# Kernel tuning notes

Measured on AMD Instinct MI355X. Metric: run time of the kernel, lower is better.

The kernel has to match this reference:

```python
import jax, jax.numpy as jnp
import numpy as np

N, M, D = 4096, 4096, 8

def laplace_tensor_markov(x, grid, lengthscale):
    # product over dims of exp(-|x_i - y_j|/ls) == exp(-sum_d |x_id - y_jd|/ls_d)
    # x: [n,d], grid: [m,d] -> [n,m]
    diff = jnp.abs(x[:, None, :] - grid[None, :, :]) / lengthscale  # [n,m,d]
    return jnp.exp(-jnp.sum(diff, axis=-1))

def setup_inputs() -> dict:
    key = jax.random.key(0)
    k1, k2, k3 = jax.random.split(key, 3)
    x = jax.random.normal(k1, (N, D), dtype=jnp.float32)
    sparse_grid = jax.random.uniform(k2, (M, D), dtype=jnp.float32)
    # inverse Cholesky factor is lower-triangular; emulate its structured sparsity
    L = jax.random.normal(k3, (M, M), dtype=jnp.float32) * 0.02
    chol_inv = jnp.tril(L) + jnp.eye(M, dtype=jnp.float32)
    lengthscale = jnp.ones((D,), dtype=jnp.float32)
    return {"x": x, "sparse_grid": sparse_grid, "chol_inv": chol_inv, "lengthscale": lengthscale}

def reference(x, sparse_grid, chol_inv, lengthscale):
    k_star = laplace_tensor_markov(x, sparse_grid, lengthscale)  # [n,m]
    phi = k_star @ chol_inv                                      # [n,m]
    return phi
```

## Files before the change

### kernel.cpp

```cpp
#include <hip/hip_runtime.h>
#include <cstdint>
#include <cstddef>

typedef unsigned short u16;
typedef __bf16 bf16x8 __attribute__((ext_vector_type(8)));
typedef float floatx4 __attribute__((ext_vector_type(4)));

#define NPTS 4096
#define MGRD 4096
#define DDIM 8

static __device__ __forceinline__ u16 f2bf(float f) {
    uint32_t u = __float_as_uint(f);
    u += 0x7fffu + ((u >> 16) & 1u);
    return (u16)(u >> 16);
}

__global__ __launch_bounds__(256) void prep_kernel(
    const float* __restrict__ x, const float* __restrict__ g,
    const float* __restrict__ ls, const float* __restrict__ B,
    u16* __restrict__ A, u16* __restrict__ Bt)
{
    __shared__ float tile[64][65];
    const int bid = blockIdx.x;
    const int tid = threadIdx.x;

    if (bid < 512) {
        const int kb = bid & 1;
        const int n0 = (bid >> 1) * 16;
        const int k0 = kb * 2048 + tid * 8;

        float il[DDIM];
#pragma unroll
        for (int d = 0; d < DDIM; ++d) il[d] = 1.0f / ls[d];

        float4 g0[8], g1[8];
#pragma unroll
        for (int r = 0; r < 8; ++r) {
            g0[r] = *reinterpret_cast<const float4*>(g + (size_t)(k0 + r) * DDIM);
            g1[r] = *reinterpret_cast<const float4*>(g + (size_t)(k0 + r) * DDIM + 4);
        }

        for (int nn = 0; nn < 16; ++nn) {
            const int n = n0 + nn;
            const float4 x0 = *reinterpret_cast<const float4*>(x + (size_t)n * DDIM);
            const float4 x1 = *reinterpret_cast<const float4*>(x + (size_t)n * DDIM + 4);
            alignas(16) u16 res[8];
#pragma unroll
            for (int r = 0; r < 8; ++r) {
                float s = fabsf(x0.x - g0[r].x) * il[0] + fabsf(x0.y - g0[r].y) * il[1]
                        + fabsf(x0.z - g0[r].z) * il[2] + fabsf(x0.w - g0[r].w) * il[3]
                        + fabsf(x1.x - g1[r].x) * il[4] + fabsf(x1.y - g1[r].y) * il[5]
                        + fabsf(x1.z - g1[r].z) * il[6] + fabsf(x1.w - g1[r].w) * il[7];
                res[r] = f2bf(__expf(-s));
            }
            *reinterpret_cast<uint4*>(A + (size_t)n * MGRD + k0) =
                *reinterpret_cast<const uint4*>(res);
        }
    } else {
        const int id = bid - 512;
        const int bx = id & 63;
        const int by = id >> 6;
        if (by < (bx & ~1)) return;
        const int k0 = by * 64;
        const int m0 = bx * 64;

#pragma unroll
        for (int r = 0; r < 4; ++r) {
            int c   = r * 256 + tid;
            int row = c >> 4;
            int col = (c & 15) * 4;
            const float4 v = *reinterpret_cast<const float4*>(&B[(size_t)(k0 + row) * MGRD + m0 + col]);
            tile[row][col + 0] = v.x; tile[row][col + 1] = v.y;
            tile[row][col + 2] = v.z; tile[row][col + 3] = v.w;
        }
        __syncthreads();

#pragma unroll
        for (int r = 0; r < 2; ++r) {
            int c  = r * 256 + tid;
            int mr = c >> 3;
            int kc = (c & 7) * 8;
            alignas(16) u16 tmp[8];
#pragma unroll
            for (int j = 0; j < 8; ++j)
                tmp[j] = f2bf(tile[kc + j][mr]);
            *reinterpret_cast<uint4*>(&Bt[(size_t)(m0 + mr) * MGRD + k0 + kc]) =
                *reinterpret_cast<const uint4*>(tmp);
        }
    }
}


#define FENCE() asm volatile("" ::: "memory")
static __device__ __forceinline__ void bar() {
    FENCE(); __builtin_amdgcn_s_barrier(); FENCE();
}

__global__ __launch_bounds__(512, 2) void gemm_pair_kernel(
    const u16* __restrict__ A,
    const u16* __restrict__ Bt,
    float* __restrict__ C)
{
    __shared__ u16 lds[3 * 24576] __attribute__((aligned(16)));

    const int tid  = threadIdx.x;
    const int lane = tid & 63;
    const int w    = tid >> 6;
    const int kg   = w >> 2;
    const int wq   = w & 3;
    const int nq   = wq >> 1;
    const int mq   = wq & 1;
    const int lrow = lane & 15;
    const int lhi  = lane >> 4;
    const int r7   = lrow & 7;

    const int id  = blockIdx.x;
    const int bm1 = id >> 4;
    const int bn  = id & 15;
    const int bn0 = bn << 8;

    const int arow = tid >> 3;
    const int aswz = ((tid ^ arow) & 7) * 8;
    int aoff[4];
#pragma unroll
    for (int r = 0; r < 4; ++r)
        aoff[r] = (bn0 + r * 64 + arow) * 4096 + aswz;

    const int ldst = w * 512;
    const int cswz = ((kg * 4 + lhi) ^ r7) * 8;
    const int rowA = (nq * 128 + lrow) * 64 + cswz;
    const int rowB = (mq * 64  + lrow) * 64 + cswz;

#define STG_A(QA, R, K) __builtin_amdgcn_global_load_lds(                        \
    (const __attribute__((address_space(1))) void*)(A + (size_t)aoff[R] + (K)),  \
    (__attribute__((address_space(3))) void*)((QA) + (R) * 4096 + ldst), 16, 0, 0)
#define STG_B(QB, R, K) __builtin_amdgcn_global_load_lds(                        \
    (const __attribute__((address_space(1))) void*)(Bt + (size_t)boff[R] + (K)), \
    (__attribute__((address_space(3))) void*)((QB) + (R) * 4096 + ldst), 16, 0, 0)

    bf16x8 af[8], bfv[4];

    floatx4 acc[8][4];

#define MF(a, b, c) __builtin_amdgcn_mfma_f32_16x16x32_bf16(a, b, c, 0, 0, 0)
#define MFMA32() do {                                                            \
    __builtin_amdgcn_s_setprio(1);                                               \
    _Pragma("unroll")                                                            \
    for (int i_ = 0; i_ < 8; ++i_)                                               \
        _Pragma("unroll")                                                        \
        for (int j_ = 0; j_ < 4; ++j_)                                           \
            acc[i_][j_] = MF(af[i_], bfv[j_], acc[i_][j_]);                      \
    __builtin_amdgcn_s_setprio(0);                                               \
} while (0)

#define REGION(PA, PB, QA, QB, KST) do {                                         \
    STG_A(QA, 0, KST); STG_A(QA, 1, KST);                                        \
    af[0]  = *reinterpret_cast<const bf16x8*>((PA) + rowA + 0 * 1024);           \
    bfv[0] = *reinterpret_cast<const bf16x8*>((PB) + rowB + 0 * 1024);           \
    bfv[1] = *reinterpret_cast<const bf16x8*>((PB) + rowB + 1 * 1024);           \
    bfv[2] = *reinterpret_cast<const bf16x8*>((PB) + rowB + 2 * 1024);           \
    bfv[3] = *reinterpret_cast<const bf16x8*>((PB) + rowB + 3 * 1024);           \
    STG_A(QA, 2, KST); STG_A(QA, 3, KST);                                        \
    af[1]  = *reinterpret_cast<const bf16x8*>((PA) + rowA + 1 * 1024);           \
    af[2]  = *reinterpret_cast<const bf16x8*>((PA) + rowA + 2 * 1024);           \
    af[3]  = *reinterpret_cast<const bf16x8*>((PA) + rowA + 3 * 1024);           \
    STG_B(QB, 0, KST); STG_B(QB, 1, KST);                                        \
    af[4]  = *reinterpret_cast<const bf16x8*>((PA) + rowA + 4 * 1024);           \
    af[5]  = *reinterpret_cast<const bf16x8*>((PA) + rowA + 5 * 1024);           \
    af[6]  = *reinterpret_cast<const bf16x8*>((PA) + rowA + 6 * 1024);           \
    af[7]  = *reinterpret_cast<const bf16x8*>((PA) + rowA + 7 * 1024);           \
    MFMA32();                                                                    \
} while (0)

#define RDALL(PA, PB) do {                                                       \
    af[0]  = *reinterpret_cast<const bf16x8*>((PA) + rowA + 0 * 1024);           \
    bfv[0] = *reinterpret_cast<const bf16x8*>((PB) + rowB + 0 * 1024);           \
    bfv[1] = *reinterpret_cast<const bf16x8*>((PB) + rowB + 1 * 1024);           \
    bfv[2] = *reinterpret_cast<const bf16x8*>((PB) + rowB + 2 * 1024);           \
    bfv[3] = *reinterpret_cast<const bf16x8*>((PB) + rowB + 3 * 1024);           \
    af[1]  = *reinterpret_cast<const bf16x8*>((PA) + rowA + 1 * 1024);           \
    af[2]  = *reinterpret_cast<const bf16x8*>((PA) + rowA + 2 * 1024);           \
    af[3]  = *reinterpret_cast<const bf16x8*>((PA) + rowA + 3 * 1024);           \
    af[4]  = *reinterpret_cast<const bf16x8*>((PA) + rowA + 4 * 1024);           \
    af[5]  = *reinterpret_cast<const bf16x8*>((PA) + rowA + 5 * 1024);           \
    af[6]  = *reinterpret_cast<const bf16x8*>((PA) + rowA + 6 * 1024);           \
    af[7]  = *reinterpret_cast<const bf16x8*>((PA) + rowA + 7 * 1024);           \
} while (0)

    for (int jj = 0; jj < 2; ++jj) {
        const int bm  = jj ? (31 - bm1) : bm1;
        const int bm0 = bm << 7;
        const int L   = 64 - 2 * bm;

        int boff[2];
#pragma unroll
        for (int r = 0; r < 2; ++r)
            boff[r] = (bm0 + r * 64 + arow) * 4096 + aswz;

#pragma unroll
        for (int i = 0; i < 8; ++i)
#pragma unroll
            for (int j = 0; j < 4; ++j)
                acc[i][j] = (floatx4)0.0f;

        int kT = 4096 - 64;
        {
            u16* qA0 = lds;             u16* qB0 = lds + 16384;
            u16* qA1 = lds + 24576;     u16* qB1 = lds + 24576 + 16384;
            STG_A(qA0, 0, kT); STG_A(qA0, 1, kT); STG_A(qA0, 2, kT); STG_A(qA0, 3, kT);
            STG_B(qB0, 0, kT); STG_B(qB0, 1, kT);
            STG_A(qA1, 0, kT - 64); STG_A(qA1, 1, kT - 64);
            STG_A(qA1, 2, kT - 64); STG_A(qA1, 3, kT - 64);
            STG_B(qB1, 0, kT - 64); STG_B(qB1, 1, kT - 64);
        }
        asm volatile("s_waitcnt vmcnt(6)" ::: "memory");
        bar();

        int p = 0;
        for (int T = 0; T < L - 2; ++T) {
            u16* pA = lds + p * 24576;  u16* pB = pA + 16384;
            int p2 = p + 2; if (p2 >= 3) p2 -= 3;
            u16* qA = lds + p2 * 24576; u16* qB = qA + 16384;

            REGION(pA, pB, qA, qB, kT - 128);
            asm volatile("s_waitcnt vmcnt(6)" ::: "memory");
            bar();

            kT -= 64; ++p; if (p == 3) p = 0;
        }

        {
            u16* pA = lds + p * 24576;  u16* pB = pA + 16384;
            RDALL(pA, pB);
            MFMA32();
            asm volatile("s_waitcnt vmcnt(0)" ::: "memory");
            bar();
            ++p; if (p == 3) p = 0;
        }
        {
            u16* pA = lds + p * 24576;  u16* pB = pA + 16384;
            RDALL(pA, pB);
            MFMA32();
        }

        __syncthreads();
        float* scr = reinterpret_cast<float*>(lds);
        if (kg == 1) {
#pragma unroll
            for (int i = 0; i < 8; ++i)
#pragma unroll
                for (int j = 0; j < 4; ++j)
                    *reinterpret_cast<floatx4*>(
                        scr + (size_t)wq * 8192 + (i * 4 + j) * 256 + lane * 4) = acc[i][j];
        }
        __syncthreads();
        if (kg == 0) {
#pragma unroll
            for (int i = 0; i < 8; ++i)
#pragma unroll
                for (int j = 0; j < 4; ++j)
                    acc[i][j] += *reinterpret_cast<const floatx4*>(
                        scr + (size_t)wq * 8192 + (i * 4 + j) * 256 + lane * 4);

#pragma unroll
            for (int i = 0; i < 8; ++i) {
                int rown = bn0 + nq * 128 + i * 16 + lhi * 4;
#pragma unroll
                for (int j = 0; j < 4; ++j) {
                    int colm = bm0 + mq * 64 + j * 16 + lrow;
                    float* cp = C + (size_t)rown * 4096 + colm;
#pragma unroll
                    for (int rr = 0; rr < 4; ++rr)
                        cp[(size_t)rr * 4096] = acc[i][j][rr];
                }
            }
        }
        __syncthreads();
    }
}

extern "C" void kernel_launch(void* const* d_in, const int* in_sizes, int n_in,
                              void* d_out, int out_size, void* d_ws, size_t ws_size,
                              hipStream_t stream)
{
    const float* x    = (const float*)d_in[0];
    const float* grid = (const float*)d_in[1];
    const float* ci   = (const float*)d_in[2];
    const float* ls   = (const float*)d_in[3];
    float* out = (float*)d_out;

    u16* wsA  = (u16*)d_ws;
    u16* wsBt = (u16*)d_ws + (size_t)MGRD * MGRD;

    prep_kernel<<<dim3(512 + 64 * 64), 256, 0, stream>>>(x, grid, ls, ci, wsA, wsBt);
    gemm_pair_kernel<<<dim3(256), 512, 0, stream>>>(wsA, wsBt, out);
}
```

Measured before the change: 185.1 us.

## Fuse prep and GEMM into one cooperative persistent kernel with grid sync

```diff
diff --git a/kernel.cpp b/kernel.cpp
--- a/kernel.cpp
+++ b/kernel.cpp
@@ -1,6 +1,9 @@
 #include <hip/hip_runtime.h>
+#include <hip/hip_cooperative_groups.h>
 #include <cstdint>
 #include <cstddef>
+
+namespace cg = cooperative_groups;
 
 typedef unsigned short u16;
 typedef __bf16 bf16x8 __attribute__((ext_vector_type(8)));
@@ -9,6 +12,9 @@
 #define NPTS 4096
 #define MGRD 4096
 #define DDIM 8
+
+#define AS1 __attribute__((address_space(1)))
+#define AS3 __attribute__((address_space(3)))
 
 static __device__ __forceinline__ u16 f2bf(float f) {
     uint32_t u = __float_as_uint(f);
@@ -16,19 +22,32 @@
     return (u16)(u >> 16);
 }
 
-__global__ __launch_bounds__(256) void prep_kernel(
-    const float* __restrict__ x, const float* __restrict__ g,
-    const float* __restrict__ ls, const float* __restrict__ B,
-    u16* __restrict__ A, u16* __restrict__ Bt)
+#define FENCE() asm volatile("" ::: "memory")
+static __device__ __forceinline__ void bar() {
+    FENCE(); __builtin_amdgcn_s_barrier(); FENCE();
+}
+
+
+__global__ __launch_bounds__(512, 2) void mega_kernel(
+    const float* __restrict__ x,
+    const float* __restrict__ g,
+    const float* __restrict__ ls,
+    const float* __restrict__ B,
+    u16* __restrict__ A,
+    u16* __restrict__ Bt,
+    float* __restrict__ C)
 {
-    __shared__ float tile[64][65];
+    __shared__ u16 lds[3 * 24576] __attribute__((aligned(16)));
+
     const int bid = blockIdx.x;
     const int tid = threadIdx.x;
 
-    if (bid < 512) {
-        const int kb = bid & 1;
-        const int n0 = (bid >> 1) * 16;
-        const int k0 = kb * 2048 + tid * 8;
+    {
+        const int vb = bid * 2 + (tid >> 8);
+        const int t  = tid & 255;
+        const int kb = vb & 1;
+        const int n0 = (vb >> 1) * 16;
+        const int k0 = kb * 2048 + t * 8;
 
         float il[DDIM];
 #pragma unroll
@@ -57,54 +76,54 @@
             *reinterpret_cast<uint4*>(A + (size_t)n * MGRD + k0) =
                 *reinterpret_cast<const uint4*>(res);
         }
-    } else {
-        const int id = bid - 512;
-        const int bx = id & 63;
-        const int by = id >> 6;
-        if (by < (bx & ~1)) return;
-        const int k0 = by * 64;
-        const int m0 = bx * 64;
-
-#pragma unroll
-        for (int r = 0; r < 4; ++r) {
-            int c   = r * 256 + tid;
-            int row = c >> 4;
-            int col = (c & 15) * 4;
-            const float4 v = *reinterpret_cast<const float4*>(&B[(size_t)(k0 + row) * MGRD + m0 + col]);
-            tile[row][col + 0] = v.x; tile[row][col + 1] = v.y;
-            tile[row][col + 2] = v.z; tile[row][col + 3] = v.w;
-        }
-        __syncthreads();
-
-#pragma unroll
-        for (int r = 0; r < 2; ++r) {
-            int c  = r * 256 + tid;
-            int mr = c >> 3;
-            int kc = (c & 7) * 8;
-            alignas(16) u16 tmp[8];
-#pragma unroll
-            for (int j = 0; j < 8; ++j)
-                tmp[j] = f2bf(tile[kc + j][mr]);
-            *reinterpret_cast<uint4*>(&Bt[(size_t)(m0 + mr) * MGRD + k0 + kc]) =
-                *reinterpret_cast<const uint4*>(tmp);
-        }
     }
-}
-
-
-#define FENCE() asm volatile("" ::: "memory")
-static __device__ __forceinline__ void bar() {
-    FENCE(); __builtin_amdgcn_s_barrier(); FENCE();
-}
-
-__global__ __launch_bounds__(512, 2) void gemm_pair_kernel(
-    const u16* __restrict__ A,
-    const u16* __restrict__ Bt,
-    float* __restrict__ C)
-{
-    __shared__ u16 lds[3 * 24576] __attribute__((aligned(16)));
-
-    const int tid  = threadIdx.x;
+
+    {
+        float* tf = reinterpret_cast<float*>(lds) + (tid >> 8) * 4160;
+        const int t = tid & 255;
+#pragma unroll 1
+        for (int r = 0; r < 8; ++r) {
+            const int idt = bid * 16 + r * 2 + (tid >> 8);
+            const int bx = idt & 63;
+            const int by = idt >> 6;
+            const bool act = (by >= (bx & ~1));
+            const int k0 = by * 64;
+            const int m0 = bx * 64;
+
+            __syncthreads();
+            if (act) {
+#pragma unroll
+                for (int rr = 0; rr < 4; ++rr) {
+                    int c   = rr * 256 + t;
+                    int row = c >> 4;
+                    int col = (c & 15) * 4;
+                    const float4 v = *reinterpret_cast<const float4*>(
+                        &B[(size_t)(k0 + row) * MGRD + m0 + col]);
+                    tf[row * 65 + col + 0] = v.x; tf[row * 65 + col + 1] = v.y;
+                    tf[row * 65 + col + 2] = v.z; tf[row * 65 + col + 3] = v.w;
+                }
+            }
+            __syncthreads();
+            if (act) {
+#pragma unroll
+                for (int rr = 0; rr < 2; ++rr) {
+                    int c  = rr * 256 + t;
+                    int mr = c >> 3;
+                    int kc = (c & 7) * 8;
+                    alignas(16) u16 tmp[8];
+#pragma unroll
+                    for (int j = 0; j < 8; ++j)
+                        tmp[j] = f2bf(tf[(kc + j) * 65 + mr]);
+                    *reinterpret_cast<uint4*>(&Bt[(size_t)(m0 + mr) * MGRD + k0 + kc]) =
+                        *reinterpret_cast<const uint4*>(tmp);
+                }
+            }
+        }
+    }
+
+    __threadfence();
+    cg::this_grid().sync();
+
     const int lane = tid & 63;
     const int w    = tid >> 6;
     const int kg   = w >> 2;
@@ -115,7 +134,7 @@
     const int lhi  = lane >> 4;
     const int r7   = lrow & 7;
 
-    const int id  = blockIdx.x;
+    const int id  = bid;
     const int bm1 = id >> 4;
     const int bn  = id & 15;
     const int bn0 = bn << 8;
@@ -133,14 +152,13 @@
     const int rowB = (mq * 64  + lrow) * 64 + cswz;
 
 #define STG_A(QA, R, K) __builtin_amdgcn_global_load_lds(                        \
-    (const __attribute__((address_space(1))) void*)(A + (size_t)aoff[R] + (K)),  \
-    (__attribute__((address_space(3))) void*)((QA) + (R) * 4096 + ldst), 16, 0, 0)
+    (const AS1 void*)(A + (size_t)aoff[R] + (K)),                                \
+    (AS3 void*)((QA) + (R) * 4096 + ldst), 16, 0, 0)
 #define STG_B(QB, R, K) __builtin_amdgcn_global_load_lds(                        \
-    (const __attribute__((address_space(1))) void*)(Bt + (size_t)boff[R] + (K)), \
-    (__attribute__((address_space(3))) void*)((QB) + (R) * 4096 + ldst), 16, 0, 0)
+    (const AS1 void*)(Bt + (size_t)boff[R] + (K)),                               \
+    (AS3 void*)((QB) + (R) * 4096 + ldst), 16, 0, 0)
 
     bf16x8 af[8], bfv[4];
-
     floatx4 acc[8][4];
 
 #define MF(a, b, c) __builtin_amdgcn_mfma_f32_16x16x32_bf16(a, b, c, 0, 0, 0)
@@ -293,6 +311,15 @@
     u16* wsA  = (u16*)d_ws;
     u16* wsBt = (u16*)d_ws + (size_t)MGRD * MGRD;
 
-    prep_kernel<<<dim3(512 + 64 * 64), 256, 0, stream>>>(x, grid, ls, ci, wsA, wsBt);
-    gemm_pair_kernel<<<dim3(256), 512, 0, stream>>>(wsA, wsBt, out);
+    void* args[7];
+    args[0] = (void*)&x;
+    args[1] = (void*)&grid;
+    args[2] = (void*)&ls;
+    args[3] = (void*)&ci;
+    args[4] = (void*)&wsA;
+    args[5] = (void*)&wsBt;
+    args[6] = (void*)&out;
+
+    hipLaunchCooperativeKernel((const void*)mega_kernel, dim3(256), dim3(512),
+                               args, 0, stream);
 }
```

Result: slower. 309.9 us (+67.5%).
